# Optimization experiments

Measured on AMD Instinct MI355X. Metric: run time of the kernel, lower is better.

## Reference

```python
import jax, jax.numpy as jnp
import numpy as np

B, P, C = 64, 8732, 81
NEG_POS_RATIO = 3


def _smooth_l1_masked_sum(p, t, maskf):
    # smooth_l1 with beta=1, sum reduction, restricted to positive priors
    d = jnp.abs(p - t)
    l = jnp.where(d < 1.0, 0.5 * d * d, d - 0.5)  # [B,P,K]
    return jnp.sum(l.sum(-1) * maskf)


def setup_inputs() -> dict:
    key = jax.random.key(0)
    ks = jax.random.split(key, 6)
    loc_data = jax.random.normal(ks[0], (B, P, 4), jnp.float32)
    conf_data = jax.random.normal(ks[1], (B, P, C), jnp.float32)
    four_corners_data = jax.random.normal(ks[2], (B, P, 8), jnp.float32)
    loc_t = jax.random.normal(ks[3], (B, P, 4), jnp.float32)
    four_corners_t = jax.random.normal(ks[4], (B, P, 8), jnp.float32)
    conf_t = jax.random.randint(ks[5], (B, P), 0, C, jnp.int32)
    return {
        "loc_data": loc_data,
        "conf_data": conf_data,
        "four_corners_data": four_corners_data,
        "loc_t": loc_t,
        "four_corners_t": four_corners_t,
        "conf_t": conf_t,
    }


def reference(loc_data, conf_data, four_corners_data, loc_t, four_corners_t, conf_t):
    num_priors = conf_data.shape[1]
    pos = conf_t > 0                                  # [B,P]
    posf = pos.astype(conf_data.dtype)

    # localization + four-corner smooth-L1 over matched (positive) priors
    loss_l = _smooth_l1_masked_sum(loc_data, loc_t, posf)
    loss_four_corners = _smooth_l1_masked_sum(four_corners_data, four_corners_t, posf)

    # per-prior CE loss: log_sum_exp(conf) - conf[target]
    lse = jax.nn.logsumexp(conf_data, axis=-1)        # [B,P]
    gathered = jnp.take_along_axis(conf_data, conf_t[..., None], axis=-1)[..., 0]
    ce_all = lse - gathered                           # [B,P]

    # hard-negative mining: rank negatives by CE loss (double argsort)
    loss_c_mine = jnp.where(pos, 0.0, ce_all)
    loss_idx = jnp.argsort(-loss_c_mine, axis=1)      # descending sort indices
    idx_rank = jnp.argsort(loss_idx, axis=1)          # rank of each prior
    num_pos = pos.sum(axis=1, keepdims=True)          # [B,1]
    num_neg = jnp.minimum(NEG_POS_RATIO * num_pos, num_priors - 1)
    neg = idx_rank < num_neg                          # [B,P]

    sel = pos | neg
    loss_c = jnp.sum(jnp.where(sel, ce_all, 0.0))

    N = num_pos.sum().astype(conf_data.dtype)
    return (loss_l / N, loss_c / N, loss_four_corners / N)
```

## Files before the change

kernel.cpp:

```cpp
#include <hip/hip_runtime.h>


#define NB 64
#define NP 8732
#define NC 81
constexpr int BP   = NB * NP;
constexpr int NQ   = BP / 4;
constexpr int NT   = NQ * 2;
constexpr int NBLK = NT / 64;
constexpr int QPB  = NP / 4;

__device__ inline float sl1(float d) {
    d = fabsf(d);
    return d < 1.0f ? 0.5f * d * d : d - 0.5f;
}
__device__ inline float e4(float4 v) {
    return __expf(v.x) + __expf(v.y) + __expf(v.z) + __expf(v.w);
}

__global__ void k_init(float* z) {
    z[threadIdx.x] = 0.0f;
}

__global__ __launch_bounds__(64) void k_main(
    const float* __restrict__ loc_data, const float* __restrict__ conf_data,
    const float* __restrict__ fc_data,  const float* __restrict__ loc_t,
    const float* __restrict__ fc_t,     const int* __restrict__ conf_t,
    float* __restrict__ ce, float* __restrict__ acc,
    float* __restrict__ spos_b, float* __restrict__ sneg_b, float* __restrict__ npf_b)
{
    const int lane = threadIdx.x;
    const int tid  = blockIdx.x * 64 + lane;
    const int q    = tid >> 1;
    const int h    = tid & 1;

    const float4* cf = (const float4*)conf_data + (size_t)q * 81;
    float s0 = 0.f, s1 = 0.f, s2 = 0.f, s3 = 0.f;
    if (h == 0) {
        float4 v;
        #pragma unroll 10
        for (int k = 0; k < 20; ++k) { v = cf[k]; s0 += e4(v); }
        v = cf[20];
        s0 += __expf(v.x); s1 += __expf(v.y) + __expf(v.z) + __expf(v.w);
        #pragma unroll 10
        for (int k = 21; k < 40; ++k) { v = cf[k]; s1 += e4(v); }
        v = cf[40];
        s1 += __expf(v.x) + __expf(v.y); s2 += __expf(v.z) + __expf(v.w);
    } else {
        float4 v;
        #pragma unroll 10
        for (int k = 41; k < 60; ++k) { v = cf[k]; s2 += e4(v); }
        v = cf[60];
        s2 += __expf(v.x) + __expf(v.y) + __expf(v.z); s3 += __expf(v.w);
        #pragma unroll 10
        for (int k = 61; k < 81; ++k) { v = cf[k]; s3 += e4(v); }
    }
    s0 += __shfl_xor(s0, 1, 64);
    s1 += __shfl_xor(s1, 1, 64);
    s2 += __shfl_xor(s2, 1, 64);
    s3 += __shfl_xor(s3, 1, 64);

    const size_t rA = (size_t)4 * q + 2 * h;
    const int2 tg = *(const int2*)(conf_t + rA);
    const float sA = h ? s2 : s0;
    const float sB = h ? s3 : s1;
    const float ceA = __logf(sA) - conf_data[rA * NC + tg.x];
    const float ceB = __logf(sB) - conf_data[(rA + 1) * NC + tg.y];
    *(float2*)(ce + rA) = make_float2(ceA, ceB);
    float sp = (tg.x > 0 ? ceA : 0.f) + (tg.y > 0 ? ceB : 0.f);
    float sn = (ceA + ceB) - sp;
    float np = (float)((tg.x > 0) + (tg.y > 0));

    float l_acc = 0.f, f_acc = 0.f;
    #pragma unroll
    for (int j = 0; j < 2; ++j) {
        const int i = tid + j * NT;
        float4 a = ((const float4*)loc_data)[i];
        float4 b = ((const float4*)loc_t)[i];
        float m = (conf_t[i] > 0) ? 1.f : 0.f;
        l_acc += m * (sl1(a.x - b.x) + sl1(a.y - b.y) + sl1(a.z - b.z) + sl1(a.w - b.w));
    }
    #pragma unroll
    for (int j = 0; j < 4; ++j) {
        const int i = tid + j * NT;
        float4 a = ((const float4*)fc_data)[i];
        float4 b = ((const float4*)fc_t)[i];
        float m = (conf_t[i >> 1] > 0) ? 1.f : 0.f;
        f_acc += m * (sl1(a.x - b.x) + sl1(a.y - b.y) + sl1(a.z - b.z) + sl1(a.w - b.w));
    }

    const int b_ = q / QPB;
    const int b0 = __shfl(b_, 0, 64);
    const int bL = __shfl(b_, 63, 64);
    const float m0 = (b_ == b0) ? 1.f : 0.f;
    float sp0 = sp * m0, sp1 = sp - sp0;
    float sn0 = sn * m0, sn1 = sn - sn0;
    float np0 = np * m0, np1 = np - np0;
    #pragma unroll
    for (int o = 32; o; o >>= 1) {
        l_acc += __shfl_xor(l_acc, o, 64);
        f_acc += __shfl_xor(f_acc, o, 64);
        sp0 += __shfl_xor(sp0, o, 64);
        sp1 += __shfl_xor(sp1, o, 64);
        sn0 += __shfl_xor(sn0, o, 64);
        sn1 += __shfl_xor(sn1, o, 64);
        np0 += __shfl_xor(np0, o, 64);
        np1 += __shfl_xor(np1, o, 64);
    }
    if (lane == 0) {
        const int slot = blockIdx.x & 31;
        atomicAdd(&acc[slot],      l_acc);
        atomicAdd(&acc[32 + slot], f_acc);
        atomicAdd(&spos_b[b0], sp0);
        atomicAdd(&sneg_b[b0], sn0);
        atomicAdd(&npf_b[b0],  np0);
        if (bL != b0) {
            atomicAdd(&spos_b[bL], sp1);
            atomicAdd(&sneg_b[bL], sn1);
            atomicAdd(&npf_b[bL],  np1);
        }
    }
}

__global__ __launch_bounds__(256) void k_batch(
    const float* __restrict__ ce, const int* __restrict__ conf_t,
    const float* __restrict__ npf_b, const float* __restrict__ spos_b,
    const float* __restrict__ sneg_b, float* __restrict__ loss_c_b)
{
    const int b = blockIdx.x;
    const int t = threadIdx.x;
    const int npos    = (int)(npf_b[b] + 0.5f);
    const int nneg    = NP - npos;
    const int num_neg = min(3 * npos, NP - 1);

    if (num_neg >= nneg) {
        if (t == 0) loss_c_b[b] = spos_b[b] + sneg_b[b];
        return;
    }
    if (num_neg <= 0) {
        if (t == 0) loss_c_b[b] = spos_b[b];
        return;
    }

    __shared__ float ce_s[NP];
    __shared__ float sredf[4];
    __shared__ int   sredi[4];
    const float* crow = ce + (size_t)b * NP;
    const int*   trow = conf_t + (size_t)b * NP;
    for (int p = t; p < NP; p += 256)
        ce_s[p] = (trow[p] > 0) ? -1.0f : crow[p];
    __syncthreads();

    const int wave = t >> 6, lane = t & 63;
    const int K = num_neg;
    unsigned lo = 0u, hi = 0x7f800000u;
    while (lo < hi) {
        unsigned mid = lo + ((hi - lo) >> 1);
        float v = __uint_as_float(mid);
        int c_t = 0;
        for (int p = t; p < NP; p += 256) c_t += (ce_s[p] > v) ? 1 : 0;
        #pragma unroll
        for (int o = 32; o; o >>= 1) c_t += __shfl_xor(c_t, o, 64);
        __syncthreads();
        if (lane == 0) sredi[wave] = c_t;
        __syncthreads();
        int cnt = sredi[0] + sredi[1] + sredi[2] + sredi[3];
        if (cnt < K) hi = mid; else lo = mid + 1;
    }
    float v = __uint_as_float(lo);
    int c_t = 0; float s_t = 0.0f;
    for (int p = t; p < NP; p += 256) {
        float x = ce_s[p];
        if (x > v) { c_t++; s_t += x; }
    }
    #pragma unroll
    for (int o = 32; o; o >>= 1) {
        c_t += __shfl_xor(c_t, o, 64);
        s_t += __shfl_xor(s_t, o, 64);
    }
    __syncthreads();
    if (lane == 0) { sredi[wave] = c_t; sredf[wave] = s_t; }
    __syncthreads();
    if (t == 0) {
        int   cnt = sredi[0] + sredi[1] + sredi[2] + sredi[3];
        float sgt = sredf[0] + sredf[1] + sredf[2] + sredf[3];
        loss_c_b[b] = spos_b[b] + sgt + (float)(K - cnt) * v;
    }
}

__global__ void k_final(const float* __restrict__ acc,
                        const float* __restrict__ loss_c_b,
                        const float* __restrict__ npf_b,
                        float* __restrict__ out)
{
    const int t = threadIdx.x;
    const float av = acc[t];
    float a0 = (t < 32) ? av : 0.0f;
    float a1 = av - a0;
    float lc = loss_c_b[t];
    float np = npf_b[t];
    #pragma unroll
    for (int o = 32; o; o >>= 1) {
        a0 += __shfl_xor(a0, o, 64);
        a1 += __shfl_xor(a1, o, 64);
        lc += __shfl_xor(lc, o, 64);
        np += __shfl_xor(np, o, 64);
    }
    if (t == 0) {
        out[0] = a0 / np;
        out[1] = lc / np;
        out[2] = a1 / np;
    }
}

extern "C" void kernel_launch(void* const* d_in, const int* in_sizes, int n_in,
                              void* d_out, int out_size, void* d_ws, size_t ws_size,
                              hipStream_t stream)
{
    const float* loc_data  = (const float*)d_in[0];
    const float* conf_data = (const float*)d_in[1];
    const float* fc_data   = (const float*)d_in[2];
    const float* loc_t     = (const float*)d_in[3];
    const float* fc_t      = (const float*)d_in[4];
    const int*   conf_t    = (const int*)d_in[5];
    float* out = (float*)d_out;

    float* ce       = (float*)d_ws;
    float* acc      = ce + BP;
    float* spos_b   = acc + 64;
    float* sneg_b   = spos_b + 64;
    float* npf_b    = sneg_b + 64;
    float* loss_c_b = npf_b + 64;

    hipLaunchKernelGGL(k_init,  dim3(1),    dim3(256), 0, stream, acc);
    hipLaunchKernelGGL(k_main,  dim3(NBLK), dim3(64),  0, stream,
                       loc_data, conf_data, fc_data, loc_t, fc_t, conf_t,
                       ce, acc, spos_b, sneg_b, npf_b);
    hipLaunchKernelGGL(k_batch, dim3(NB),   dim3(256), 0, stream,
                       ce, conf_t, npf_b, spos_b, sneg_b, loss_c_b);
    hipLaunchKernelGGL(k_final, dim3(1),    dim3(64),  0, stream,
                       acc, loss_c_b, npf_b, out);
}
```

Measured before the change: 322.0 us.

## Stage conf rows through LDS with coalesced loads in a persistent grid

Result: slower. 444.1 us (+37.9%).

```diff
diff --git a/kernel.cpp b/kernel.cpp
--- a/kernel.cpp
+++ b/kernel.cpp
@@ -4,141 +4,123 @@
 #define NB 64
 #define NP 8732
 #define NC 81
-constexpr int BP   = NB * NP;
-constexpr int NQ   = BP / 4;
-constexpr int NT   = NQ * 2;
-constexpr int NBLK = NT / 64;
-constexpr int QPB  = NP / 4;
+constexpr int BP     = NB * NP;
+constexpr int NTILES = BP / 64;
+constexpr int GRID   = 2048;
+constexpr int BLK    = 512;
+constexpr int TOTTHR = GRID * BLK;
 
 __device__ inline float sl1(float d) {
     d = fabsf(d);
     return d < 1.0f ? 0.5f * d * d : d - 0.5f;
 }
-__device__ inline float e4(float4 v) {
-    return __expf(v.x) + __expf(v.y) + __expf(v.z) + __expf(v.w);
-}
 
 __global__ void k_init(float* z) {
     z[threadIdx.x] = 0.0f;
 }
 
-__global__ __launch_bounds__(64) void k_main(
+__global__ __launch_bounds__(BLK, 8) void k_main(
     const float* __restrict__ loc_data, const float* __restrict__ conf_data,
     const float* __restrict__ fc_data,  const float* __restrict__ loc_t,
     const float* __restrict__ fc_t,     const int* __restrict__ conf_t,
-    float* __restrict__ ce, float* __restrict__ acc,
-    float* __restrict__ spos_b, float* __restrict__ sneg_b, float* __restrict__ npf_b)
-{
-    const int lane = threadIdx.x;
-    const int tid  = blockIdx.x * 64 + lane;
-    const int q    = tid >> 1;
-    const int h    = tid & 1;
-
-    const float4* cf = (const float4*)conf_data + (size_t)q * 81;
-    float s0 = 0.f, s1 = 0.f, s2 = 0.f, s3 = 0.f;
-    if (h == 0) {
-        float4 v;
-        #pragma unroll 10
-        for (int k = 0; k < 20; ++k) { v = cf[k]; s0 += e4(v); }
-        v = cf[20];
-        s0 += __expf(v.x); s1 += __expf(v.y) + __expf(v.z) + __expf(v.w);
-        #pragma unroll 10
-        for (int k = 21; k < 40; ++k) { v = cf[k]; s1 += e4(v); }
-        v = cf[40];
-        s1 += __expf(v.x) + __expf(v.y); s2 += __expf(v.z) + __expf(v.w);
-    } else {
-        float4 v;
-        #pragma unroll 10
-        for (int k = 41; k < 60; ++k) { v = cf[k]; s2 += e4(v); }
-        v = cf[60];
-        s2 += __expf(v.x) + __expf(v.y) + __expf(v.z); s3 += __expf(v.w);
-        #pragma unroll 10
-        for (int k = 61; k < 81; ++k) { v = cf[k]; s3 += e4(v); }
-    }
-    s0 += __shfl_xor(s0, 1, 64);
-    s1 += __shfl_xor(s1, 1, 64);
-    s2 += __shfl_xor(s2, 1, 64);
-    s3 += __shfl_xor(s3, 1, 64);
-
-    const size_t rA = (size_t)4 * q + 2 * h;
-    const int2 tg = *(const int2*)(conf_t + rA);
-    const float sA = h ? s2 : s0;
-    const float sB = h ? s3 : s1;
-    const float ceA = __logf(sA) - conf_data[rA * NC + tg.x];
-    const float ceB = __logf(sB) - conf_data[(rA + 1) * NC + tg.y];
-    *(float2*)(ce + rA) = make_float2(ceA, ceB);
-    float sp = (tg.x > 0 ? ceA : 0.f) + (tg.y > 0 ? ceB : 0.f);
-    float sn = (ceA + ceB) - sp;
-    float np = (float)((tg.x > 0) + (tg.y > 0));
-
-    float l_acc = 0.f, f_acc = 0.f;
-    #pragma unroll
-    for (int j = 0; j < 2; ++j) {
-        const int i = tid + j * NT;
+    float* __restrict__ ce, float* __restrict__ acc, float* __restrict__ gb)
+{
+    __shared__ float conf_s[64 * NC];
+    __shared__ int   tgt_s[64];
+    __shared__ float lds_acc[192];
+
+    const int t    = threadIdx.x;
+    const int lane = t & 63;
+    const int gtid = blockIdx.x * BLK + t;
+
+    if (t < 192) lds_acc[t] = 0.0f;
+
+    for (int tile = blockIdx.x; tile < NTILES; tile += GRID) {
+        const float4* src = (const float4*)conf_data + (size_t)tile * 1296;
+        #pragma unroll
+        for (int k = 0; k < 3; ++k) {
+            const int i = k * BLK + t;
+            if (i < 1296) ((float4*)conf_s)[i] = src[i];
+        }
+        if (t < 16) ((int4*)tgt_s)[t] = ((const int4*)(conf_t + tile * 64))[t];
+        __syncthreads();
+
+        const int r = t >> 3;
+        const int o = t & 7;
+        const float* rowp = conf_s + r * NC;
+        const float* cp = rowp + o * 10;
+        float s = 0.0f;
+        #pragma unroll
+        for (int j = 0; j < 10; ++j) s += __expf(cp[j]);
+        if (o == 7) s += __expf(rowp[80]);
+        s += __shfl_xor(s, 1, 64);
+        s += __shfl_xor(s, 2, 64);
+        s += __shfl_xor(s, 4, 64);
+        if (o == 0) {
+            const int row = tile * 64 + r;
+            const int tgt = tgt_s[r];
+            const float cev = __logf(s) - rowp[tgt];
+            ce[row] = cev;
+            const int b = row / NP;
+            if (tgt > 0) {
+                atomicAdd(&lds_acc[b], cev);
+                atomicAdd(&lds_acc[128 + b], 1.0f);
+            } else {
+                atomicAdd(&lds_acc[64 + b], cev);
+            }
+        }
+        __syncthreads();
+    }
+
+    float l_acc = 0.0f, f_acc = 0.0f;
+    for (int i = gtid; i < BP; i += TOTTHR) {
         float4 a = ((const float4*)loc_data)[i];
         float4 b = ((const float4*)loc_t)[i];
-        float m = (conf_t[i] > 0) ? 1.f : 0.f;
+        float m = (conf_t[i] > 0) ? 1.0f : 0.0f;
         l_acc += m * (sl1(a.x - b.x) + sl1(a.y - b.y) + sl1(a.z - b.z) + sl1(a.w - b.w));
     }
-    #pragma unroll
-    for (int j = 0; j < 4; ++j) {
-        const int i = tid + j * NT;
+    for (int i = gtid; i < 2 * BP; i += TOTTHR) {
         float4 a = ((const float4*)fc_data)[i];
         float4 b = ((const float4*)fc_t)[i];
-        float m = (conf_t[i >> 1] > 0) ? 1.f : 0.f;
+        float m = (conf_t[i >> 1] > 0) ? 1.0f : 0.0f;
         f_acc += m * (sl1(a.x - b.x) + sl1(a.y - b.y) + sl1(a.z - b.z) + sl1(a.w - b.w));
     }
-
-    const int b_ = q / QPB;
-    const int b0 = __shfl(b_, 0, 64);
-    const int bL = __shfl(b_, 63, 64);
-    const float m0 = (b_ == b0) ? 1.f : 0.f;
-    float sp0 = sp * m0, sp1 = sp - sp0;
-    float sn0 = sn * m0, sn1 = sn - sn0;
-    float np0 = np * m0, np1 = np - np0;
     #pragma unroll
-    for (int o = 32; o; o >>= 1) {
-        l_acc += __shfl_xor(l_acc, o, 64);
-        f_acc += __shfl_xor(f_acc, o, 64);
-        sp0 += __shfl_xor(sp0, o, 64);
-        sp1 += __shfl_xor(sp1, o, 64);
-        sn0 += __shfl_xor(sn0, o, 64);
-        sn1 += __shfl_xor(sn1, o, 64);
-        np0 += __shfl_xor(np0, o, 64);
-        np1 += __shfl_xor(np1, o, 64);
+    for (int o2 = 32; o2; o2 >>= 1) {
+        l_acc += __shfl_xor(l_acc, o2, 64);
+        f_acc += __shfl_xor(f_acc, o2, 64);
     }
     if (lane == 0) {
         const int slot = blockIdx.x & 31;
         atomicAdd(&acc[slot],      l_acc);
         atomicAdd(&acc[32 + slot], f_acc);
-        atomicAdd(&spos_b[b0], sp0);
-        atomicAdd(&sneg_b[b0], sn0);
-        atomicAdd(&npf_b[b0],  np0);
-        if (bL != b0) {
-            atomicAdd(&spos_b[bL], sp1);
-            atomicAdd(&sneg_b[bL], sn1);
-            atomicAdd(&npf_b[bL],  np1);
-        }
+    }
+
+    __syncthreads();
+    if (t < 192) {
+        float v = lds_acc[t];
+        if (v != 0.0f) atomicAdd(&gb[t], v);
     }
 }
 
 __global__ __launch_bounds__(256) void k_batch(
     const float* __restrict__ ce, const int* __restrict__ conf_t,
-    const float* __restrict__ npf_b, const float* __restrict__ spos_b,
-    const float* __restrict__ sneg_b, float* __restrict__ loss_c_b)
+    const float* __restrict__ gb, float* __restrict__ loss_c_b)
 {
     const int b = blockIdx.x;
     const int t = threadIdx.x;
-    const int npos    = (int)(npf_b[b] + 0.5f);
+    const float spos = gb[b];
+    const float sneg = gb[64 + b];
+    const int npos    = (int)(gb[128 + b] + 0.5f);
     const int nneg    = NP - npos;
     const int num_neg = min(3 * npos, NP - 1);
 
     if (num_neg >= nneg) {
-        if (t == 0) loss_c_b[b] = spos_b[b] + sneg_b[b];
+        if (t == 0) loss_c_b[b] = spos + sneg;
         return;
     }
     if (num_neg <= 0) {
-        if (t == 0) loss_c_b[b] = spos_b[b];
+        if (t == 0) loss_c_b[b] = spos;
         return;
     }
 
@@ -184,13 +166,13 @@
     if (t == 0) {
         int   cnt = sredi[0] + sredi[1] + sredi[2] + sredi[3];
         float sgt = sredf[0] + sredf[1] + sredf[2] + sredf[3];
-        loss_c_b[b] = spos_b[b] + sgt + (float)(K - cnt) * v;
+        loss_c_b[b] = spos + sgt + (float)(K - cnt) * v;
     }
 }
 
 __global__ void k_final(const float* __restrict__ acc,
+                        const float* __restrict__ gb,
                         const float* __restrict__ loss_c_b,
-                        const float* __restrict__ npf_b,
                         float* __restrict__ out)
 {
     const int t = threadIdx.x;
@@ -198,7 +180,7 @@
     float a0 = (t < 32) ? av : 0.0f;
     float a1 = av - a0;
     float lc = loss_c_b[t];
-    float np = npf_b[t];
+    float np = gb[128 + t];
     #pragma unroll
     for (int o = 32; o; o >>= 1) {
         a0 += __shfl_xor(a0, o, 64);
@@ -227,17 +209,15 @@
 
     float* ce       = (float*)d_ws;
     float* acc      = ce + BP;
-    float* spos_b   = acc + 64;
-    float* sneg_b   = spos_b + 64;
-    float* npf_b    = sneg_b + 64;
-    float* loss_c_b = npf_b + 64;
+    float* gb       = acc + 64;
+    float* loss_c_b = gb + 192;
 
     hipLaunchKernelGGL(k_init,  dim3(1),    dim3(256), 0, stream, acc);
-    hipLaunchKernelGGL(k_main,  dim3(NBLK), dim3(64),  0, stream,
+    hipLaunchKernelGGL(k_main,  dim3(GRID), dim3(BLK), 0, stream,
                        loc_data, conf_data, fc_data, loc_t, fc_t, conf_t,
-                       ce, acc, spos_b, sneg_b, npf_b);
+                       ce, acc, gb);
     hipLaunchKernelGGL(k_batch, dim3(NB),   dim3(256), 0, stream,
-                       ce, conf_t, npf_b, spos_b, sneg_b, loss_c_b);
+                       ce, conf_t, gb, loss_c_b);
     hipLaunchKernelGGL(k_final, dim3(1),    dim3(64),  0, stream,
-                       acc, loss_c_b, npf_b, out);
-}
+                       acc, gb, loss_c_b, out);
+}
```
